# Kernel tuning notes

Hardware: AMD Instinct MI355X
Metric: run time of the kernel (lower is better)

## Reference

```python
import jax, jax.numpy as jnp
import numpy as np

NU = 0.01 / np.pi  # viscosity buffer from the torch module


def _mlp(x, W_in, b_in, W_hid, b_hid, W_out, b_out):
    # x: [N, 2] -> u: [N, 1]; tanh MLP with stacked hidden layers scanned.
    h = jnp.tanh(x @ W_in + b_in)

    def step(h, wb):
        W, b = wb
        return jnp.tanh(h @ W + b), None

    h, _ = jax.lax.scan(step, h, (W_hid, b_hid))
    return h @ W_out + b_out


def setup_inputs() -> dict:
    key = jax.random.key(0)
    ks = jax.random.split(key, 10)
    N_f, N0, Nb, H, L = 131072, 4096, 2048, 128, 7
    s_in = 1.0 / np.sqrt(2.0)
    s_h = 1.0 / np.sqrt(H)
    return {
        "x_f": jax.random.normal(ks[0], (N_f, 2), jnp.float32),
        "x0_cat": jax.random.normal(ks[1], (N0, 2), jnp.float32),
        "xb_left_cat": jax.random.normal(ks[2], (Nb, 2), jnp.float32),
        "xb_right_cat": jax.random.normal(ks[3], (Nb, 2), jnp.float32),
        "W_in": jax.random.normal(ks[4], (2, H), jnp.float32) * s_in,
        "b_in": jax.random.normal(ks[5], (H,), jnp.float32) * 0.01,
        "W_hid": jax.random.normal(ks[6], (L, H, H), jnp.float32) * s_h,
        "b_hid": jax.random.normal(ks[7], (L, H), jnp.float32) * 0.01,
        "W_out": jax.random.normal(ks[8], (H, 1), jnp.float32) * s_h,
        "b_out": jax.random.normal(ks[9], (1,), jnp.float32) * 0.01,
    }


def reference(x_f, x0_cat, xb_left_cat, xb_right_cat,
              W_in, b_in, W_hid, b_hid, W_out, b_out):
    u = lambda x: _mlp(x, W_in, b_in, W_hid, b_hid, W_out, b_out)

    u_0_pred = u(x0_cat)
    u_b_left_pred = u(xb_left_cat)
    u_b_right_pred = u(xb_right_cat)

    u_f_pred = u(x_f)  # [N_f, 1]

    # Each row of u depends only on the matching row of x, so grad of the sum
    # yields per-example gradients (equivalent to torch.autograd.grad with
    # grad_outputs=ones).
    usum = lambda x: u(x).sum()
    g = jax.grad(usum)(x_f)            # [N_f, 2]
    u_x = g[:, 0:1]
    u_t = g[:, 1:2]

    # Second derivative: grad of sum(u_x) w.r.t. x, take the x-component.
    uxx_full = jax.grad(lambda x: jax.grad(usum)(x)[:, 0].sum())(x_f)
    u_xx = uxx_full[:, 0:1]

    pde_residual = u_t + u_f_pred * u_x - NU * u_xx
    return jnp.concatenate((u_0_pred, u_b_left_pred, u_b_right_pred,
                            pde_residual), axis=0)
```

## Files before the change

### kernel.cpp

```cpp
#include <hip/hip_runtime.h>
#include <math.h>

#define NU_F 0.0031830988618379067f
#define KTANH 2.885390082f

typedef _Float16 f16x8 __attribute__((ext_vector_type(8)));
typedef float    f32x4 __attribute__((ext_vector_type(4)));

__device__ __forceinline__ float tanh_pre(float zs) {
    float e = __builtin_amdgcn_exp2f(zs);
    float r = __builtin_amdgcn_rcpf(e + 1.0f);
    return fmaf(-2.0f, r, 1.0f);
}

__device__ __forceinline__ unsigned pkf16(float a, float b) {
    auto v = __builtin_amdgcn_cvt_pkrtz(a, b);
    return __builtin_bit_cast(unsigned, v);
}

__global__ void prep_wfrag(const float* __restrict__ Whid, _Float16* __restrict__ wcf)
{
    const int t    = blockIdx.x * 256 + threadIdx.x;
    const int lane = t & 63;
    const int fid  = t >> 6;
    const int ks = fid & 3;
    const int nt = (fid >> 2) & 7;
    const int l  = fid >> 5;
    const int q  = lane >> 4;
    const int nn = lane & 15;
    const int c  = ((nt >> 1) << 5) + nn * 2 + (nt & 1);
    const int k0 = ks * 32 + q * 8;
    const float* src = Whid + l * 16384 + k0 * 128 + c;
    f16x8 v;
    #pragma unroll
    for (int jj = 0; jj < 8; ++jj)
        v[jj] = (_Float16)src[jj * 128];
    *(f16x8*)(wcf + (size_t)t * 8) = v;
}

#define HR 68
#define MFMA(A, B, C) __builtin_amdgcn_mfma_f32_16x16x32_f16((A), (B), (C), 0, 0, 0)

__global__ __launch_bounds__(256, 4)
void pinn_fused(const float* __restrict__ xf,
                const float* __restrict__ x0,  const float* __restrict__ xbl,
                const float* __restrict__ xbr,
                const float* __restrict__ Win,  const float* __restrict__ bin,
                const float* __restrict__ bhid,
                const float* __restrict__ Wout, const float* __restrict__ bout,
                const _Float16* __restrict__ wcf,
                float* __restrict__ out)
{
    __shared__ unsigned Hh[64 * HR];
    __shared__ float xpt[128];
    __shared__ float pbuf[256];
    __shared__ float dots[64];

    const int tid  = threadIdx.x;
    const int lane = tid & 63;
    const int wv   = tid >> 6;
    const int lm   = lane & 15;
    const int lq   = lane >> 4;
    const int blk  = blockIdx.x;
    const bool isv = (blk >= 8192);

    if (!isv) {
        if (tid < 32) xpt[tid] = xf[blk * 32 + tid];
    } else {
        if (tid < 128) {
            const int vb = blk - 8192;
            const float* src = (vb < 64) ? (x0 + vb * 128)
                             : (vb < 96) ? (xbl + (vb - 64) * 128)
                                         : (xbr + (vb - 96) * 128);
            xpt[tid] = src[tid];
        }
    }
    __syncthreads();

    const int cp = tid & 63;
    {
        const float2 w01 = *(const float2*)&Win[cp * 2];
        const float2 w11 = *(const float2*)&Win[128 + cp * 2];
        const float2 bb  = *(const float2*)&bin[cp * 2];
        const float w01sx = w01.x * KTANH, w01sy = w01.y * KTANH;
        const float w11sx = w11.x * KTANH, w11sy = w11.y * KTANH;
        const float bbsx  = bb.x  * KTANH, bbsy  = bb.y  * KTANH;
        if (!isv) {
            const int p0 = wv * 4;
            #pragma unroll
            for (int i = 0; i < 4; ++i) {
                const int p = p0 + i;
                const float x = xpt[2 * p], tt = xpt[2 * p + 1];
                const float ya = tanh_pre(fmaf(x, w01sx, fmaf(tt, w11sx, bbsx)));
                const float yb = tanh_pre(fmaf(x, w01sy, fmaf(tt, w11sy, bbsy)));
                const float da = 1.f - ya * ya, db = 1.f - yb * yb;
                Hh[(0 * 16 + p) * HR + cp] = pkf16(ya, yb);
                Hh[(1 * 16 + p) * HR + cp] = pkf16(da * w01.x, db * w01.y);
                Hh[(2 * 16 + p) * HR + cp] = pkf16(da * w11.x, db * w11.y);
                Hh[(3 * 16 + p) * HR + cp] =
                    pkf16(-2.f * ya * da * w01.x * w01.x,
                          -2.f * yb * db * w01.y * w01.y);
            }
        } else {
            const int p0 = wv * 16;
            #pragma unroll
            for (int i = 0; i < 16; ++i) {
                const int p = p0 + i;
                const float x = xpt[2 * p], tt = xpt[2 * p + 1];
                const float ya = tanh_pre(fmaf(x, w01sx, fmaf(tt, w11sx, bbsx)));
                const float yb = tanh_pre(fmaf(x, w01sy, fmaf(tt, w11sy, bbsy)));
                Hh[p * HR + cp] = pkf16(ya, yb);
            }
        }
    }
    __syncthreads();

    const _Float16* pb0 = wcf + (wv * 2 + 0) * 2048 + lane * 8;
    const _Float16* pb1 = wcf + (wv * 2 + 1) * 2048 + lane * 8;
    const int wc = wv * 16 + lm;

    if (!isv) {
        for (int l = 0; l < 7; ++l) {
            float bbs[2];
            {
                const float2 bt = *(const float2*)&bhid[l * 128 + wv * 32 + lm * 2];
                bbs[0] = bt.x * KTANH; bbs[1] = bt.y * KTANH;
            }

            f32x4 acc[4][2];
            #pragma unroll
            for (int s = 0; s < 4; ++s)
                #pragma unroll
                for (int j = 0; j < 2; ++j) acc[s][j] = (f32x4){0.f, 0.f, 0.f, 0.f};

            #pragma unroll
            for (int ks = 0; ks < 4; ++ks) {
                const int ro = ks * 16 + lq * 4;
                const f16x8 ah0 = *(const f16x8*)&Hh[(0 * 16 + lm) * HR + ro];
                const f16x8 ah1 = *(const f16x8*)&Hh[(1 * 16 + lm) * HR + ro];
                const f16x8 ah2 = *(const f16x8*)&Hh[(2 * 16 + lm) * HR + ro];
                const f16x8 ah3 = *(const f16x8*)&Hh[(3 * 16 + lm) * HR + ro];
                const f16x8 b0 = *(const f16x8*)(pb0 + ks * 512);
                const f16x8 b1 = *(const f16x8*)(pb1 + ks * 512);
                acc[0][0] = MFMA(ah0, b0, acc[0][0]);
                acc[1][0] = MFMA(ah1, b0, acc[1][0]);
                acc[2][0] = MFMA(ah2, b0, acc[2][0]);
                acc[3][0] = MFMA(ah3, b0, acc[3][0]);
                acc[0][1] = MFMA(ah0, b1, acc[0][1]);
                acc[1][1] = MFMA(ah1, b1, acc[1][1]);
                acc[2][1] = MFMA(ah2, b1, acc[2][1]);
                acc[3][1] = MFMA(ah3, b1, acc[3][1]);
            }
            __syncthreads();

            #pragma unroll
            for (int r = 0; r < 4; ++r) {
                const int p = lq * 4 + r;
                float h[2][4];
                #pragma unroll
                for (int j = 0; j < 2; ++j) {
                    const float zx  = acc[1][j][r];
                    const float zt  = acc[2][j][r];
                    const float zxx = acc[3][j][r];
                    const float y = tanh_pre(fmaf(acc[0][j][r], KTANH, bbs[j]));
                    const float d = fmaf(-y, y, 1.f);
                    const float m = d * zx;
                    h[j][0] = y;
                    h[j][1] = m;
                    h[j][2] = d * zt;
                    h[j][3] = fmaf(d, zxx, -2.f * (y * m) * zx);
                }
                #pragma unroll
                for (int s = 0; s < 4; ++s)
                    Hh[(s * 16 + p) * HR + wc] = pkf16(h[0][s], h[1][s]);
            }
            pb0 += 16384; pb1 += 16384;
            __syncthreads();
        }
    } else {
        for (int l = 0; l < 7; ++l) {
            float bbs[2];
            {
                const float2 bt = *(const float2*)&bhid[l * 128 + wv * 32 + lm * 2];
                bbs[0] = bt.x * KTANH; bbs[1] = bt.y * KTANH;
            }

            f32x4 acc[4][2];
            #pragma unroll
            for (int mt = 0; mt < 4; ++mt)
                #pragma unroll
                for (int j = 0; j < 2; ++j) acc[mt][j] = (f32x4){0.f, 0.f, 0.f, 0.f};

            #pragma unroll
            for (int ks = 0; ks < 4; ++ks) {
                const int ro = ks * 16 + lq * 4;
                f16x8 ah[4];
                #pragma unroll
                for (int mt = 0; mt < 4; ++mt)
                    ah[mt] = *(const f16x8*)&Hh[(mt * 16 + lm) * HR + ro];
                const f16x8 b0 = *(const f16x8*)(pb0 + ks * 512);
                const f16x8 b1 = *(const f16x8*)(pb1 + ks * 512);
                #pragma unroll
                for (int mt = 0; mt < 4; ++mt) {
                    acc[mt][0] = MFMA(ah[mt], b0, acc[mt][0]);
                    acc[mt][1] = MFMA(ah[mt], b1, acc[mt][1]);
                }
            }
            __syncthreads();

            #pragma unroll
            for (int mt = 0; mt < 4; ++mt) {
                #pragma unroll
                for (int r = 0; r < 4; ++r) {
                    const int p = mt * 16 + lq * 4 + r;
                    const float y0 = tanh_pre(fmaf(acc[mt][0][r], KTANH, bbs[0]));
                    const float y1 = tanh_pre(fmaf(acc[mt][1][r], KTANH, bbs[1]));
                    Hh[p * HR + wc] = pkf16(y0, y1);
                }
            }
            pb0 += 16384; pb1 += 16384;
            __syncthreads();
        }
    }

    {
        const int st = lane;
        const int ch = wv;
        const int cb = ch * 16;
        float part = 0.f;
        #pragma unroll
        for (int c8 = 0; c8 < 4; ++c8) {
            const f16x8 hv = *(const f16x8*)&Hh[st * HR + cb + c8 * 4];
            const float4 w1 = *(const float4*)&Wout[ch * 32 + c8 * 8];
            const float4 w2 = *(const float4*)&Wout[ch * 32 + c8 * 8 + 4];
            part = fmaf((float)hv[0], w1.x, part);
            part = fmaf((float)hv[1], w1.y, part);
            part = fmaf((float)hv[2], w1.z, part);
            part = fmaf((float)hv[3], w1.w, part);
            part = fmaf((float)hv[4], w2.x, part);
            part = fmaf((float)hv[5], w2.y, part);
            part = fmaf((float)hv[6], w2.z, part);
            part = fmaf((float)hv[7], w2.w, part);
        }
        pbuf[ch * 64 + st] = part;
    }
    __syncthreads();
    if (tid < 64)
        dots[tid] = (pbuf[tid] + pbuf[64 + tid]) + (pbuf[128 + tid] + pbuf[192 + tid]);
    __syncthreads();
    if (!isv) {
        if (tid < 16) {
            const float u = dots[tid] + bout[0];
            out[8192 + blk * 16 + tid] =
                dots[32 + tid] + u * dots[16 + tid] - NU_F * dots[48 + tid];
        }
    } else {
        if (tid < 64) out[(blk - 8192) * 64 + tid] = dots[tid] + bout[0];
    }
}

extern "C" void kernel_launch(void* const* d_in, const int* in_sizes, int n_in,
                              void* d_out, int out_size, void* d_ws, size_t ws_size,
                              hipStream_t stream) {
    (void)in_sizes; (void)n_in; (void)ws_size; (void)out_size;
    const float* xf   = (const float*)d_in[0];
    const float* x0   = (const float*)d_in[1];
    const float* xbl  = (const float*)d_in[2];
    const float* xbr  = (const float*)d_in[3];
    const float* Win  = (const float*)d_in[4];
    const float* bin  = (const float*)d_in[5];
    const float* Whid = (const float*)d_in[6];
    const float* bhid = (const float*)d_in[7];
    const float* Wout = (const float*)d_in[8];
    const float* bout = (const float*)d_in[9];
    float* out = (float*)d_out;

    _Float16* wcf = (_Float16*)d_ws;

    hipLaunchKernelGGL(prep_wfrag, dim3(14336 / 256), dim3(256), 0, stream,
                       Whid, wcf);
    hipLaunchKernelGGL(pinn_fused, dim3(8192 + 128), dim3(256), 0, stream,
                       xf, x0, xbl, xbr, Win, bin, bhid, Wout, bout, wcf, out);
}
```

Measured before the change: 219.4 us.

## Switch hidden-layer GEMMs to 32x32x16 MFMA with double-buffered LDS activations

Replaces the 16x16x32 MFMA tiling with 32x32x16 MFMA. Each wave now computes a 32-row by 64-column tile, and the weight fragments are re-packed to match. The activation buffer in shared memory is double-buffered, which removes one __syncthreads per layer. Rows are interleaved by derivative stream (point*4+stream) and the final reduction remaps the order back. The aim is fewer MFMA issues and fewer LDS A-fragment reloads, at the cost of more shared memory and larger accumulator register use, which may lower occupancy.

```diff
diff --git a/kernel.cpp b/kernel.cpp
--- a/kernel.cpp
+++ b/kernel.cpp
@@ -4,8 +4,9 @@
 #define NU_F 0.0031830988618379067f
 #define KTANH 2.885390082f
 
-typedef _Float16 f16x8 __attribute__((ext_vector_type(8)));
-typedef float    f32x4 __attribute__((ext_vector_type(4)));
+typedef _Float16 f16x8  __attribute__((ext_vector_type(8)));
+typedef float    f32x4  __attribute__((ext_vector_type(4)));
+typedef float    f32x16 __attribute__((ext_vector_type(16)));
 
 __device__ __forceinline__ float tanh_pre(float zs) {
     float e = __builtin_amdgcn_exp2f(zs);
@@ -22,15 +23,15 @@
 {
     const int t    = blockIdx.x * 256 + threadIdx.x;
     const int lane = t & 63;
-    const int fid  = t >> 6;
-    const int ks = fid & 3;
-    const int nt = (fid >> 2) & 7;
-    const int l  = fid >> 5;
-    const int q  = lane >> 4;
-    const int nn = lane & 15;
-    const int c  = ((nt >> 1) << 5) + nn * 2 + (nt & 1);
-    const int k0 = ks * 32 + q * 8;
-    const float* src = Whid + l * 16384 + k0 * 128 + c;
+    const int f    = t >> 6;
+    const int ks = f & 7;
+    const int nt = (f >> 3) & 3;
+    const int l  = f >> 5;
+    const int n  = lane & 31;
+    const int hi = lane >> 5;
+    const int ch = ((nt >> 1) << 6) + n * 2 + (nt & 1);
+    const int kk = ks * 16 + hi * 8;
+    const float* src = Whid + l * 16384 + kk * 128 + ch;
     f16x8 v;
     #pragma unroll
     for (int jj = 0; jj < 8; ++jj)
@@ -38,8 +39,8 @@
     *(f16x8*)(wcf + (size_t)t * 8) = v;
 }
 
-#define HR 68
-#define MFMA(A, B, C) __builtin_amdgcn_mfma_f32_16x16x32_f16((A), (B), (C), 0, 0, 0)
+#define RS 68
+#define MFMA32(A, B, C) __builtin_amdgcn_mfma_f32_32x32x16_f16((A), (B), (C), 0, 0, 0)
 
 __global__ __launch_bounds__(256, 4)
 void pinn_fused(const float* __restrict__ xf,
@@ -51,7 +52,7 @@
                 const _Float16* __restrict__ wcf,
                 float* __restrict__ out)
 {
-    __shared__ unsigned Hh[64 * HR];
+    __shared__ unsigned Hh[2][64 * RS];
     __shared__ float xpt[128];
     __shared__ float pbuf[256];
     __shared__ float dots[64];
@@ -59,8 +60,11 @@
     const int tid  = threadIdx.x;
     const int lane = tid & 63;
     const int wv   = tid >> 6;
-    const int lm   = lane & 15;
-    const int lq   = lane >> 4;
+    const int nl   = lane & 31;
+    const int hi   = lane >> 5;
+    const int mt   = wv & 1;
+    const int ntp  = wv >> 1;
+    const int cdw  = ntp * 32 + nl;
     const int blk  = blockIdx.x;
     const bool isv = (blk >= 8192);
 
@@ -94,10 +98,10 @@
                 const float ya = tanh_pre(fmaf(x, w01sx, fmaf(tt, w11sx, bbsx)));
                 const float yb = tanh_pre(fmaf(x, w01sy, fmaf(tt, w11sy, bbsy)));
                 const float da = 1.f - ya * ya, db = 1.f - yb * yb;
-                Hh[(0 * 16 + p) * HR + cp] = pkf16(ya, yb);
-                Hh[(1 * 16 + p) * HR + cp] = pkf16(da * w01.x, db * w01.y);
-                Hh[(2 * 16 + p) * HR + cp] = pkf16(da * w11.x, db * w11.y);
-                Hh[(3 * 16 + p) * HR + cp] =
+                Hh[0][(p * 4 + 0) * RS + cp] = pkf16(ya, yb);
+                Hh[0][(p * 4 + 1) * RS + cp] = pkf16(da * w01.x, db * w01.y);
+                Hh[0][(p * 4 + 2) * RS + cp] = pkf16(da * w11.x, db * w11.y);
+                Hh[0][(p * 4 + 3) * RS + cp] =
                     pkf16(-2.f * ya * da * w01.x * w01.x,
                           -2.f * yb * db * w01.y * w01.y);
             }
@@ -109,114 +113,91 @@
                 const float x = xpt[2 * p], tt = xpt[2 * p + 1];
                 const float ya = tanh_pre(fmaf(x, w01sx, fmaf(tt, w11sx, bbsx)));
                 const float yb = tanh_pre(fmaf(x, w01sy, fmaf(tt, w11sy, bbsy)));
-                Hh[p * HR + cp] = pkf16(ya, yb);
-            }
-        }
-    }
-    __syncthreads();
-
-    const _Float16* pb0 = wcf + (wv * 2 + 0) * 2048 + lane * 8;
-    const _Float16* pb1 = wcf + (wv * 2 + 1) * 2048 + lane * 8;
-    const int wc = wv * 16 + lm;
+                Hh[0][p * RS + cp] = pkf16(ya, yb);
+            }
+        }
+    }
+    __syncthreads();
+
+    const _Float16* pb0 = wcf + ntp * 8192 + lane * 8;
+    const _Float16* pb1 = pb0 + 4096;
+    const int arow = (mt * 32 + nl) * RS + hi * 4;
 
     if (!isv) {
         for (int l = 0; l < 7; ++l) {
-            float bbs[2];
-            {
-                const float2 bt = *(const float2*)&bhid[l * 128 + wv * 32 + lm * 2];
-                bbs[0] = bt.x * KTANH; bbs[1] = bt.y * KTANH;
-            }
-
-            f32x4 acc[4][2];
-            #pragma unroll
-            for (int s = 0; s < 4; ++s)
-                #pragma unroll
-                for (int j = 0; j < 2; ++j) acc[s][j] = (f32x4){0.f, 0.f, 0.f, 0.f};
-
-            #pragma unroll
-            for (int ks = 0; ks < 4; ++ks) {
-                const int ro = ks * 16 + lq * 4;
-                const f16x8 ah0 = *(const f16x8*)&Hh[(0 * 16 + lm) * HR + ro];
-                const f16x8 ah1 = *(const f16x8*)&Hh[(1 * 16 + lm) * HR + ro];
-                const f16x8 ah2 = *(const f16x8*)&Hh[(2 * 16 + lm) * HR + ro];
-                const f16x8 ah3 = *(const f16x8*)&Hh[(3 * 16 + lm) * HR + ro];
-                const f16x8 b0 = *(const f16x8*)(pb0 + ks * 512);
-                const f16x8 b1 = *(const f16x8*)(pb1 + ks * 512);
-                acc[0][0] = MFMA(ah0, b0, acc[0][0]);
-                acc[1][0] = MFMA(ah1, b0, acc[1][0]);
-                acc[2][0] = MFMA(ah2, b0, acc[2][0]);
-                acc[3][0] = MFMA(ah3, b0, acc[3][0]);
-                acc[0][1] = MFMA(ah0, b1, acc[0][1]);
-                acc[1][1] = MFMA(ah1, b1, acc[1][1]);
-                acc[2][1] = MFMA(ah2, b1, acc[2][1]);
-                acc[3][1] = MFMA(ah3, b1, acc[3][1]);
-            }
-            __syncthreads();
-
-            #pragma unroll
-            for (int r = 0; r < 4; ++r) {
-                const int p = lq * 4 + r;
-                float h[2][4];
-                #pragma unroll
-                for (int j = 0; j < 2; ++j) {
-                    const float zx  = acc[1][j][r];
-                    const float zt  = acc[2][j][r];
-                    const float zxx = acc[3][j][r];
-                    const float y = tanh_pre(fmaf(acc[0][j][r], KTANH, bbs[j]));
+            const unsigned* Hc = Hh[l & 1];
+            unsigned*       Hn = Hh[(l & 1) ^ 1];
+            const float2 bt = *(const float2*)&bhid[l * 128 + ntp * 64 + nl * 2];
+            const float bbs0 = bt.x * KTANH, bbs1 = bt.y * KTANH;
+
+            f32x16 a0, a1;
+            #pragma unroll
+            for (int i = 0; i < 16; ++i) { a0[i] = 0.f; a1[i] = 0.f; }
+
+            #pragma unroll
+            for (int ks = 0; ks < 8; ++ks) {
+                const f16x8 A  = *(const f16x8*)&Hc[arow + ks * 8];
+                const f16x8 B0 = *(const f16x8*)(pb0 + ks * 512);
+                const f16x8 B1 = *(const f16x8*)(pb1 + ks * 512);
+                a0 = MFMA32(A, B0, a0);
+                a1 = MFMA32(A, B1, a1);
+            }
+
+            #pragma unroll
+            for (int q = 0; q < 4; ++q) {
+                float h0[4], h1[4];
+                {
+                    const float zx = a0[q * 4 + 1], zt = a0[q * 4 + 2],
+                                zxx = a0[q * 4 + 3];
+                    const float y = tanh_pre(fmaf(a0[q * 4 + 0], KTANH, bbs0));
                     const float d = fmaf(-y, y, 1.f);
                     const float m = d * zx;
-                    h[j][0] = y;
-                    h[j][1] = m;
-                    h[j][2] = d * zt;
-                    h[j][3] = fmaf(d, zxx, -2.f * (y * m) * zx);
+                    h0[0] = y; h0[1] = m; h0[2] = d * zt;
+                    h0[3] = fmaf(d, zxx, -2.f * (y * m) * zx);
                 }
+                {
+                    const float zx = a1[q * 4 + 1], zt = a1[q * 4 + 2],
+                                zxx = a1[q * 4 + 3];
+                    const float y = tanh_pre(fmaf(a1[q * 4 + 0], KTANH, bbs1));
+                    const float d = fmaf(-y, y, 1.f);
+                    const float m = d * zx;
+                    h1[0] = y; h1[1] = m; h1[2] = d * zt;
+                    h1[3] = fmaf(d, zxx, -2.f * (y * m) * zx);
+                }
+                const int rbase = mt * 32 + q * 8 + hi * 4;
                 #pragma unroll
                 for (int s = 0; s < 4; ++s)
-                    Hh[(s * 16 + p) * HR + wc] = pkf16(h[0][s], h[1][s]);
+                    Hn[(rbase + s) * RS + cdw] = pkf16(h0[s], h1[s]);
             }
             pb0 += 16384; pb1 += 16384;
             __syncthreads();
         }
     } else {
         for (int l = 0; l < 7; ++l) {
-            float bbs[2];
-            {
-                const float2 bt = *(const float2*)&bhid[l * 128 + wv * 32 + lm * 2];
-                bbs[0] = bt.x * KTANH; bbs[1] = bt.y * KTANH;
-            }
-
-            f32x4 acc[4][2];
-            #pragma unroll
-            for (int mt = 0; mt < 4; ++mt)
-                #pragma unroll
-                for (int j = 0; j < 2; ++j) acc[mt][j] = (f32x4){0.f, 0.f, 0.f, 0.f};
-
-            #pragma unroll
-            for (int ks = 0; ks < 4; ++ks) {
-                const int ro = ks * 16 + lq * 4;
-                f16x8 ah[4];
-                #pragma unroll
-                for (int mt = 0; mt < 4; ++mt)
-                    ah[mt] = *(const f16x8*)&Hh[(mt * 16 + lm) * HR + ro];
-                const f16x8 b0 = *(const f16x8*)(pb0 + ks * 512);
-                const f16x8 b1 = *(const f16x8*)(pb1 + ks * 512);
-                #pragma unroll
-                for (int mt = 0; mt < 4; ++mt) {
-                    acc[mt][0] = MFMA(ah[mt], b0, acc[mt][0]);
-                    acc[mt][1] = MFMA(ah[mt], b1, acc[mt][1]);
-                }
-            }
-            __syncthreads();
-
-            #pragma unroll
-            for (int mt = 0; mt < 4; ++mt) {
-                #pragma unroll
-                for (int r = 0; r < 4; ++r) {
-                    const int p = mt * 16 + lq * 4 + r;
-                    const float y0 = tanh_pre(fmaf(acc[mt][0][r], KTANH, bbs[0]));
-                    const float y1 = tanh_pre(fmaf(acc[mt][1][r], KTANH, bbs[1]));
-                    Hh[p * HR + wc] = pkf16(y0, y1);
-                }
+            const unsigned* Hc = Hh[l & 1];
+            unsigned*       Hn = Hh[(l & 1) ^ 1];
+            const float2 bt = *(const float2*)&bhid[l * 128 + ntp * 64 + nl * 2];
+            const float bbs0 = bt.x * KTANH, bbs1 = bt.y * KTANH;
+
+            f32x16 a0, a1;
+            #pragma unroll
+            for (int i = 0; i < 16; ++i) { a0[i] = 0.f; a1[i] = 0.f; }
+
+            #pragma unroll
+            for (int ks = 0; ks < 8; ++ks) {
+                const f16x8 A  = *(const f16x8*)&Hc[arow + ks * 8];
+                const f16x8 B0 = *(const f16x8*)(pb0 + ks * 512);
+                const f16x8 B1 = *(const f16x8*)(pb1 + ks * 512);
+                a0 = MFMA32(A, B0, a0);
+                a1 = MFMA32(A, B1, a1);
+            }
+
+            #pragma unroll
+            for (int r = 0; r < 16; ++r) {
+                const float y0 = tanh_pre(fmaf(a0[r], KTANH, bbs0));
+                const float y1 = tanh_pre(fmaf(a1[r], KTANH, bbs1));
+                const int row = mt * 32 + (r & 3) + (r >> 2) * 8 + hi * 4;
+                Hn[row * RS + cdw] = pkf16(y0, y1);
             }
             pb0 += 16384; pb1 += 16384;
             __syncthreads();
@@ -225,14 +206,13 @@
 
     {
         const int st = lane;
-        const int ch = wv;
-        const int cb = ch * 16;
+        const int cb = wv * 16;
         float part = 0.f;
         #pragma unroll
         for (int c8 = 0; c8 < 4; ++c8) {
-            const f16x8 hv = *(const f16x8*)&Hh[st * HR + cb + c8 * 4];
-            const float4 w1 = *(const float4*)&Wout[ch * 32 + c8 * 8];
-            const float4 w2 = *(const float4*)&Wout[ch * 32 + c8 * 8 + 4];
+            const f16x8 hv = *(const f16x8*)&Hh[1][st * RS + cb + c8 * 4];
+            const float4 w1 = *(const float4*)&Wout[wv * 32 + c8 * 8];
+            const float4 w2 = *(const float4*)&Wout[wv * 32 + c8 * 8 + 4];
             part = fmaf((float)hv[0], w1.x, part);
             part = fmaf((float)hv[1], w1.y, part);
             part = fmaf((float)hv[2], w1.z, part);
@@ -242,11 +222,15 @@
             part = fmaf((float)hv[6], w2.z, part);
             part = fmaf((float)hv[7], w2.w, part);
         }
-        pbuf[ch * 64 + st] = part;
-    }
-    __syncthreads();
-    if (tid < 64)
-        dots[tid] = (pbuf[tid] + pbuf[64 + tid]) + (pbuf[128 + tid] + pbuf[192 + tid]);
+        pbuf[wv * 64 + st] = part;
+    }
+    __syncthreads();
+    if (tid < 64) {
+        const float sum = (pbuf[tid] + pbuf[64 + tid])
+                        + (pbuf[128 + tid] + pbuf[192 + tid]);
+        const int d = isv ? tid : ((tid & 3) * 16 + (tid >> 2));
+        dots[d] = sum;
+    }
     __syncthreads();
     if (!isv) {
         if (tid < 16) {
```

New measurement: 245.1 us. +11.7%, slower.

## Double-buffer hidden-state LDS and prefetch next layer weights to drop barriers

Applied to the files above, without the earlier changes.

Splits the shared hidden-state buffer into two ping-pong halves so each layer reads one buffer and writes the other. This removes one of the two block barriers per layer. The first weight fragment and the bias of the next layer are loaded early, overlapping global latency with the tanh epilogue. Barriers become a bare lgkmcnt wait plus s_barrier. The cost is double the LDS footprint for Hh, which may reduce occupancy, plus extra live registers for the prefetched fragments.

```diff
diff --git a/kernel.cpp b/kernel.cpp
--- a/kernel.cpp
+++ b/kernel.cpp
@@ -16,6 +16,11 @@
 __device__ __forceinline__ unsigned pkf16(float a, float b) {
     auto v = __builtin_amdgcn_cvt_pkrtz(a, b);
     return __builtin_bit_cast(unsigned, v);
+}
+
+__device__ __forceinline__ void lds_barrier() {
+    asm volatile("s_waitcnt lgkmcnt(0)" ::: "memory");
+    __builtin_amdgcn_s_barrier();
 }
 
 __global__ void prep_wfrag(const float* __restrict__ Whid, _Float16* __restrict__ wcf)
@@ -51,7 +56,7 @@
                 const _Float16* __restrict__ wcf,
                 float* __restrict__ out)
 {
-    __shared__ unsigned Hh[64 * HR];
+    __shared__ unsigned Hh[2][64 * HR];
     __shared__ float xpt[128];
     __shared__ float pbuf[256];
     __shared__ float dots[64];
@@ -75,6 +80,14 @@
             xpt[tid] = src[tid];
         }
     }
+
+    const _Float16* pb0 = wcf + (wv * 2 + 0) * 2048 + lane * 8;
+    const _Float16* pb1 = wcf + (wv * 2 + 1) * 2048 + lane * 8;
+    const float* bptr = bhid + wv * 32 + lm * 2;
+    f16x8 cB0 = *(const f16x8*)pb0;
+    f16x8 cB1 = *(const f16x8*)pb1;
+    float2 btc = *(const float2*)bptr;
+
     __syncthreads();
 
     const int cp = tid & 63;
@@ -94,10 +107,10 @@
                 const float ya = tanh_pre(fmaf(x, w01sx, fmaf(tt, w11sx, bbsx)));
                 const float yb = tanh_pre(fmaf(x, w01sy, fmaf(tt, w11sy, bbsy)));
                 const float da = 1.f - ya * ya, db = 1.f - yb * yb;
-                Hh[(0 * 16 + p) * HR + cp] = pkf16(ya, yb);
-                Hh[(1 * 16 + p) * HR + cp] = pkf16(da * w01.x, db * w01.y);
-                Hh[(2 * 16 + p) * HR + cp] = pkf16(da * w11.x, db * w11.y);
-                Hh[(3 * 16 + p) * HR + cp] =
+                Hh[0][(0 * 16 + p) * HR + cp] = pkf16(ya, yb);
+                Hh[0][(1 * 16 + p) * HR + cp] = pkf16(da * w01.x, db * w01.y);
+                Hh[0][(2 * 16 + p) * HR + cp] = pkf16(da * w11.x, db * w11.y);
+                Hh[0][(3 * 16 + p) * HR + cp] =
                     pkf16(-2.f * ya * da * w01.x * w01.x,
                           -2.f * yb * db * w01.y * w01.y);
             }
@@ -109,37 +122,48 @@
                 const float x = xpt[2 * p], tt = xpt[2 * p + 1];
                 const float ya = tanh_pre(fmaf(x, w01sx, fmaf(tt, w11sx, bbsx)));
                 const float yb = tanh_pre(fmaf(x, w01sy, fmaf(tt, w11sy, bbsy)));
-                Hh[p * HR + cp] = pkf16(ya, yb);
-            }
-        }
-    }
-    __syncthreads();
-
-    const _Float16* pb0 = wcf + (wv * 2 + 0) * 2048 + lane * 8;
-    const _Float16* pb1 = wcf + (wv * 2 + 1) * 2048 + lane * 8;
+                Hh[0][p * HR + cp] = pkf16(ya, yb);
+            }
+        }
+    }
+    lds_barrier();
+
     const int wc = wv * 16 + lm;
 
     if (!isv) {
         for (int l = 0; l < 7; ++l) {
-            float bbs[2];
+            const unsigned* Hc = Hh[l & 1];
+            unsigned*       Hn = Hh[(l & 1) ^ 1];
+            const float bbs0 = btc.x * KTANH, bbs1 = btc.y * KTANH;
+
+            f32x4 acc[4][2];
+            #pragma unroll
+            for (int s = 0; s < 4; ++s)
+                #pragma unroll
+                for (int j = 0; j < 2; ++j) acc[s][j] = (f32x4){0.f, 0.f, 0.f, 0.f};
+
             {
-                const float2 bt = *(const float2*)&bhid[l * 128 + wv * 32 + lm * 2];
-                bbs[0] = bt.x * KTANH; bbs[1] = bt.y * KTANH;
-            }
-
-            f32x4 acc[4][2];
-            #pragma unroll
-            for (int s = 0; s < 4; ++s)
-                #pragma unroll
-                for (int j = 0; j < 2; ++j) acc[s][j] = (f32x4){0.f, 0.f, 0.f, 0.f};
-
-            #pragma unroll
-            for (int ks = 0; ks < 4; ++ks) {
+                const int ro = lq * 4;
+                const f16x8 ah0 = *(const f16x8*)&Hc[(0 * 16 + lm) * HR + ro];
+                const f16x8 ah1 = *(const f16x8*)&Hc[(1 * 16 + lm) * HR + ro];
+                const f16x8 ah2 = *(const f16x8*)&Hc[(2 * 16 + lm) * HR + ro];
+                const f16x8 ah3 = *(const f16x8*)&Hc[(3 * 16 + lm) * HR + ro];
+                acc[0][0] = MFMA(ah0, cB0, acc[0][0]);
+                acc[1][0] = MFMA(ah1, cB0, acc[1][0]);
+                acc[2][0] = MFMA(ah2, cB0, acc[2][0]);
+                acc[3][0] = MFMA(ah3, cB0, acc[3][0]);
+                acc[0][1] = MFMA(ah0, cB1, acc[0][1]);
+                acc[1][1] = MFMA(ah1, cB1, acc[1][1]);
+                acc[2][1] = MFMA(ah2, cB1, acc[2][1]);
+                acc[3][1] = MFMA(ah3, cB1, acc[3][1]);
+            }
+            #pragma unroll
+            for (int ks = 1; ks < 4; ++ks) {
                 const int ro = ks * 16 + lq * 4;
-                const f16x8 ah0 = *(const f16x8*)&Hh[(0 * 16 + lm) * HR + ro];
-                const f16x8 ah1 = *(const f16x8*)&Hh[(1 * 16 + lm) * HR + ro];
-                const f16x8 ah2 = *(const f16x8*)&Hh[(2 * 16 + lm) * HR + ro];
-                const f16x8 ah3 = *(const f16x8*)&Hh[(3 * 16 + lm) * HR + ro];
+                const f16x8 ah0 = *(const f16x8*)&Hc[(0 * 16 + lm) * HR + ro];
+                const f16x8 ah1 = *(const f16x8*)&Hc[(1 * 16 + lm) * HR + ro];
+                const f16x8 ah2 = *(const f16x8*)&Hc[(2 * 16 + lm) * HR + ro];
+                const f16x8 ah3 = *(const f16x8*)&Hc[(3 * 16 + lm) * HR + ro];
                 const f16x8 b0 = *(const f16x8*)(pb0 + ks * 512);
                 const f16x8 b1 = *(const f16x8*)(pb1 + ks * 512);
                 acc[0][0] = MFMA(ah0, b0, acc[0][0]);
@@ -151,7 +175,14 @@
                 acc[2][1] = MFMA(ah2, b1, acc[2][1]);
                 acc[3][1] = MFMA(ah3, b1, acc[3][1]);
             }
-            __syncthreads();
+
+            pb0 += 16384; pb1 += 16384;
+            if (l < 6) {
+                cB0 = *(const f16x8*)pb0;
+                cB1 = *(const f16x8*)pb1;
+                btc = *(const float2*)(bptr + 128);
+                bptr += 128;
+            }
 
             #pragma unroll
             for (int r = 0; r < 4; ++r) {
@@ -162,7 +193,8 @@
                     const float zx  = acc[1][j][r];
                     const float zt  = acc[2][j][r];
                     const float zxx = acc[3][j][r];
-                    const float y = tanh_pre(fmaf(acc[0][j][r], KTANH, bbs[j]));
+                    const float y = tanh_pre(fmaf(acc[0][j][r], KTANH,
+                                                  j ? bbs1 : bbs0));
                     const float d = fmaf(-y, y, 1.f);
                     const float m = d * zx;
                     h[j][0] = y;
@@ -172,32 +204,41 @@
                 }
                 #pragma unroll
                 for (int s = 0; s < 4; ++s)
-                    Hh[(s * 16 + p) * HR + wc] = pkf16(h[0][s], h[1][s]);
-            }
-            pb0 += 16384; pb1 += 16384;
-            __syncthreads();
+                    Hn[(s * 16 + p) * HR + wc] = pkf16(h[0][s], h[1][s]);
+            }
+            lds_barrier();
         }
     } else {
         for (int l = 0; l < 7; ++l) {
-            float bbs[2];
+            const unsigned* Hc = Hh[l & 1];
+            unsigned*       Hn = Hh[(l & 1) ^ 1];
+            const float bbs0 = btc.x * KTANH, bbs1 = btc.y * KTANH;
+
+            f32x4 acc[4][2];
+            #pragma unroll
+            for (int mt = 0; mt < 4; ++mt)
+                #pragma unroll
+                for (int j = 0; j < 2; ++j) acc[mt][j] = (f32x4){0.f, 0.f, 0.f, 0.f};
+
             {
-                const float2 bt = *(const float2*)&bhid[l * 128 + wv * 32 + lm * 2];
-                bbs[0] = bt.x * KTANH; bbs[1] = bt.y * KTANH;
-            }
-
-            f32x4 acc[4][2];
-            #pragma unroll
-            for (int mt = 0; mt < 4; ++mt)
-                #pragma unroll
-                for (int j = 0; j < 2; ++j) acc[mt][j] = (f32x4){0.f, 0.f, 0.f, 0.f};
-
-            #pragma unroll
-            for (int ks = 0; ks < 4; ++ks) {
+                const int ro = lq * 4;
+                f16x8 ah[4];
+                #pragma unroll
+                for (int mt = 0; mt < 4; ++mt)
+                    ah[mt] = *(const f16x8*)&Hc[(mt * 16 + lm) * HR + ro];
+                #pragma unroll
+                for (int mt = 0; mt < 4; ++mt) {
+                    acc[mt][0] = MFMA(ah[mt], cB0, acc[mt][0]);
+                    acc[mt][1] = MFMA(ah[mt], cB1, acc[mt][1]);
+                }
+            }
+            #pragma unroll
+            for (int ks = 1; ks < 4; ++ks) {
                 const int ro = ks * 16 + lq * 4;
                 f16x8 ah[4];
                 #pragma unroll
                 for (int mt = 0; mt < 4; ++mt)
-                    ah[mt] = *(const f16x8*)&Hh[(mt * 16 + lm) * HR + ro];
+                    ah[mt] = *(const f16x8*)&Hc[(mt * 16 + lm) * HR + ro];
                 const f16x8 b0 = *(const f16x8*)(pb0 + ks * 512);
                 const f16x8 b1 = *(const f16x8*)(pb1 + ks * 512);
                 #pragma unroll
@@ -206,33 +247,38 @@
                     acc[mt][1] = MFMA(ah[mt], b1, acc[mt][1]);
                 }
             }
-            __syncthreads();
+
+            pb0 += 16384; pb1 += 16384;
+            if (l < 6) {
+                cB0 = *(const f16x8*)pb0;
+                cB1 = *(const f16x8*)pb1;
+                btc = *(const float2*)(bptr + 128);
+                bptr += 128;
+            }
 
             #pragma unroll
             for (int mt = 0; mt < 4; ++mt) {
                 #pragma unroll
                 for (int r = 0; r < 4; ++r) {
                     const int p = mt * 16 + lq * 4 + r;
-                    const float y0 = tanh_pre(fmaf(acc[mt][0][r], KTANH, bbs[0]));
-                    const float y1 = tanh_pre(fmaf(acc[mt][1][r], KTANH, bbs[1]));
-                    Hh[p * HR + wc] = pkf16(y0, y1);
+                    const float y0 = tanh_pre(fmaf(acc[mt][0][r], KTANH, bbs0));
+                    const float y1 = tanh_pre(fmaf(acc[mt][1][r], KTANH, bbs1));
+                    Hn[p * HR + wc] = pkf16(y0, y1);
                 }
             }
-            pb0 += 16384; pb1 += 16384;
-            __syncthreads();
+            lds_barrier();
         }
     }
 
     {
         const int st = lane;
-        const int ch = wv;
-        const int cb = ch * 16;
+        const int cb = wv * 16;
         float part = 0.f;
         #pragma unroll
         for (int c8 = 0; c8 < 4; ++c8) {
-            const f16x8 hv = *(const f16x8*)&Hh[st * HR + cb + c8 * 4];
-            const float4 w1 = *(const float4*)&Wout[ch * 32 + c8 * 8];
-            const float4 w2 = *(const float4*)&Wout[ch * 32 + c8 * 8 + 4];
+            const f16x8 hv = *(const f16x8*)&Hh[1][st * HR + cb + c8 * 4];
+            const float4 w1 = *(const float4*)&Wout[wv * 32 + c8 * 8];
+            const float4 w2 = *(const float4*)&Wout[wv * 32 + c8 * 8 + 4];
             part = fmaf((float)hv[0], w1.x, part);
             part = fmaf((float)hv[1], w1.y, part);
             part = fmaf((float)hv[2], w1.z, part);
@@ -242,12 +288,12 @@
             part = fmaf((float)hv[6], w2.z, part);
             part = fmaf((float)hv[7], w2.w, part);
         }
-        pbuf[ch * 64 + st] = part;
-    }
-    __syncthreads();
+        pbuf[wv * 64 + st] = part;
+    }
+    lds_barrier();
     if (tid < 64)
         dots[tid] = (pbuf[tid] + pbuf[64 + tid]) + (pbuf[128 + tid] + pbuf[192 + tid]);
-    __syncthreads();
+    lds_barrier();
     if (!isv) {
         if (tid < 16) {
             const float u = dots[tid] + bout[0];
```

After: 214.9 us. 1.02x faster.
